# Performance work log

Measured on AMD Instinct MI355X. Metric: run time of the kernel, lower is better.

Reference implementation:

```python
import jax, jax.numpy as jnp
import numpy as np


def setup_inputs() -> dict:
    key = jax.random.key(0)
    ks = jax.random.split(key, 5)
    B, C, H, W = 4, 512, 64, 64
    A = 64  # attention_features
    s = lambda fan_in: 1.0 / np.sqrt(fan_in)
    return {
        "x": jax.random.normal(ks[0], (B, C, H, W), dtype=jnp.float32),
        "Wf": jax.random.normal(ks[1], (C, A), dtype=jnp.float32) * s(C),
        "bf": jnp.zeros((A,), dtype=jnp.float32),
        "Wg": jax.random.normal(ks[2], (C, A), dtype=jnp.float32) * s(C),
        "bg": jnp.zeros((A,), dtype=jnp.float32),
        "Wh": jax.random.normal(ks[3], (C, C), dtype=jnp.float32) * s(C),
        "bh": jnp.zeros((C,), dtype=jnp.float32),
        "scale": jax.random.uniform(ks[4], (), dtype=jnp.float32),
    }


def reference(x, Wf, bf, Wg, bg, Wh, bh, scale):
    B, C, H, W = x.shape
    N = H * W

    def conv1x1(w, b):  # 1x1 conv == per-pixel matmul over channels
        return jnp.einsum('bchw,cf->bfhw', x, w) + b[None, :, None, None]

    f = conv1x1(Wf, bf)  # [B, A, H, W]
    g = conv1x1(Wg, bg)  # [B, A, H, W]
    h = conv1x1(Wh, bh)  # [B, C, H, W]

    # flatten_hw (channels_first): [B, C', H, W] -> [B, N, C']
    flat = lambda t: t.reshape(B, t.shape[1], N).transpose(0, 2, 1)
    gf = flat(g)  # [B, N, A]
    ff = flat(f)  # [B, N, A]
    hf = flat(h)  # [B, N, C]

    s = jnp.einsum('bnd,bmd->bnm', gf, ff)       # [B, N, N]
    attn = jax.nn.softmax(s, axis=-1)
    o = jnp.einsum('bnm,bmc->bnc', attn, hf)     # [B, N, C]
    # Original does a raw reshape back to x's shape (no transpose) — keep it.
    y = scale * o.reshape(x.shape) + x
    return y
```

## Files before the change

### kernel.cpp

```cpp
#include <hip/hip_runtime.h>
#include <hip/hip_bf16.h>

constexpr int BB = 4;
constexpr int C  = 512;
constexpr int A  = 64;
constexpr int N  = 4096;

typedef __attribute__((ext_vector_type(8))) short s16x8;
typedef __attribute__((ext_vector_type(4))) float f32x4;

#define MFMA_16x16x32_BF16(a, b, c) __builtin_amdgcn_mfma_f32_16x16x32_bf16((a), (b), (c), 0, 0, 0)

typedef __attribute__((address_space(3))) unsigned int lds_u32_t;
typedef const __attribute__((address_space(1))) unsigned int glb_u32_t;

__device__ __forceinline__ void gl2lds16(const void* g, void* l) {
    __builtin_amdgcn_global_load_lds((glb_u32_t*)g, (lds_u32_t*)l, 16, 0, 0);
}

__global__ __launch_bounds__(256) void k_trans(const float* __restrict__ src,
                                               __hip_bfloat16* __restrict__ dst,
                                               int K, int M) {
    __shared__ __hip_bfloat16 Ls[64][66];
    int m0 = blockIdx.x << 6, k0 = blockIdx.y << 6;
    size_t bo = (size_t)blockIdx.z * K * M;
    int t = threadIdx.x;
    int lm = t & 63, g = t >> 6;
    #pragma unroll
    for (int j = 0; j < 16; ++j) {
        int kk = j * 4 + g;
        Ls[kk][lm] = __float2bfloat16(src[bo + (size_t)(k0 + kk) * M + m0 + lm]);
    }
    __syncthreads();
    #pragma unroll
    for (int j = 0; j < 16; ++j) {
        int mm = j * 4 + g;
        dst[bo + (size_t)(m0 + mm) * K + k0 + lm] = Ls[lm][mm];
    }
}

__global__ __launch_bounds__(256) void k_trans2(const float* __restrict__ src,
                                                __hip_bfloat16* __restrict__ dhi,
                                                __hip_bfloat16* __restrict__ dlo,
                                                int K, int M) {
    __shared__ float Ls[64][65];
    int m0 = blockIdx.x << 6, k0 = blockIdx.y << 6;
    size_t bo = (size_t)blockIdx.z * K * M;
    int t = threadIdx.x;
    int lm = t & 63, g = t >> 6;
    #pragma unroll
    for (int j = 0; j < 16; ++j) {
        int kk = j * 4 + g;
        Ls[kk][lm] = src[bo + (size_t)(k0 + kk) * M + m0 + lm];
    }
    __syncthreads();
    #pragma unroll
    for (int j = 0; j < 16; ++j) {
        int mm = j * 4 + g;
        float v = Ls[lm][mm];
        __hip_bfloat16 h = __float2bfloat16(v);
        size_t idx = bo + (size_t)(m0 + mm) * K + k0 + lm;
        dhi[idx] = h;
        dlo[idx] = __float2bfloat16(v - __bfloat162float(h));
    }
}

__global__ __launch_bounds__(256) void k_fgm(const __hip_bfloat16* __restrict__ XThi, const __hip_bfloat16* __restrict__ XTlo,
                                             const __hip_bfloat16* __restrict__ WfThi, const __hip_bfloat16* __restrict__ WfTlo,
                                             const __hip_bfloat16* __restrict__ WgThi, const __hip_bfloat16* __restrict__ WgTlo,
                                             const float* __restrict__ bfv, const float* __restrict__ bgv,
                                             __hip_bfloat16* __restrict__ FFhi, __hip_bfloat16* __restrict__ FFlo,
                                             __hip_bfloat16* __restrict__ GFhi, __hip_bfloat16* __restrict__ GFlo) {
    __shared__ __align__(16) __hip_bfloat16 Ah[64 * 32], Al[64 * 32];
    __shared__ __align__(16) __hip_bfloat16 Bh[128 * 32], Bl[128 * 32];
    int r0 = blockIdx.x << 6;
    int t = threadIdx.x;
    int w = t >> 6, l = t & 63;
    int ln15 = l & 15, quad = l >> 4;
    int mh = w & 1, nh = w >> 1;

    f32x4 acc[2][4];
    #pragma unroll
    for (int mi = 0; mi < 2; ++mi)
        #pragma unroll
        for (int ni = 0; ni < 4; ++ni) acc[mi][ni] = (f32x4){0.f, 0.f, 0.f, 0.f};

    for (int kt = 0; kt < C; kt += 32) {
        {
            int row = t >> 2, seg = t & 3;
            int gseg = (seg - (row >> 1)) & 3;
            size_t go = (size_t)(r0 + row) * C + kt + gseg * 8;
            gl2lds16(XThi + go, &Ah[t * 8]);
            gl2lds16(XTlo + go, &Al[t * 8]);
        }
        #pragma unroll
        for (int j = 0; j < 2; ++j) {
            int i = j * 256 + t;
            int row = i >> 2, seg = i & 3;
            int gseg = (seg - (row >> 1)) & 3;
            size_t go = (size_t)(row & 63) * C + kt + gseg * 8;
            const __hip_bfloat16* bh = j ? WgThi : WfThi;
            const __hip_bfloat16* bl = j ? WgTlo : WfTlo;
            gl2lds16(bh + go, &Bh[i * 8]);
            gl2lds16(bl + go, &Bl[i * 8]);
        }
        __syncthreads();
        s16x8 afh[2], afl[2], bfh[4], bfl[4];
        #pragma unroll
        for (int mi = 0; mi < 2; ++mi) {
            int row = mh * 32 + mi * 16 + ln15;
            int sw = ((quad + (row >> 1)) & 3) << 3;
            afh[mi] = *(const s16x8*)&Ah[row * 32 + sw];
            afl[mi] = *(const s16x8*)&Al[row * 32 + sw];
        }
        #pragma unroll
        for (int ni = 0; ni < 4; ++ni) {
            int row = nh * 64 + ni * 16 + ln15;
            int sw = ((quad + (row >> 1)) & 3) << 3;
            bfh[ni] = *(const s16x8*)&Bh[row * 32 + sw];
            bfl[ni] = *(const s16x8*)&Bl[row * 32 + sw];
        }
        #pragma unroll
        for (int mi = 0; mi < 2; ++mi)
            #pragma unroll
            for (int ni = 0; ni < 4; ++ni) {
                acc[mi][ni] = MFMA_16x16x32_BF16(afh[mi], bfh[ni], acc[mi][ni]);
                acc[mi][ni] = MFMA_16x16x32_BF16(afl[mi], bfh[ni], acc[mi][ni]);
                acc[mi][ni] = MFMA_16x16x32_BF16(afh[mi], bfl[ni], acc[mi][ni]);
            }
        __syncthreads();
    }

    #pragma unroll
    for (int mi = 0; mi < 2; ++mi) {
        #pragma unroll
        for (int r = 0; r < 4; ++r) {
            size_t grow = (size_t)(r0 + mh * 32 + mi * 16 + quad * 4 + r) * A;
            #pragma unroll
            for (int ni = 0; ni < 4; ++ni) {
                int col = nh * 64 + ni * 16 + ln15;
                if (col < A) {
                    float v = acc[mi][ni][r] + bfv[col];
                    __hip_bfloat16 h = __float2bfloat16(v);
                    FFhi[grow + col] = h;
                    FFlo[grow + col] = __float2bfloat16(v - __bfloat162float(h));
                } else {
                    int a = col - A;
                    float v = acc[mi][ni][r] + bgv[a];
                    __hip_bfloat16 h = __float2bfloat16(v);
                    GFhi[grow + a] = h;
                    GFlo[grow + a] = __float2bfloat16(v - __bfloat162float(h));
                }
            }
        }
    }
}

__global__ __launch_bounds__(256) void k_hm(const __hip_bfloat16* __restrict__ WhT,
                                            const __hip_bfloat16* __restrict__ XT,
                                            const float* __restrict__ bhv,
                                            __hip_bfloat16* __restrict__ HFT) {
    __shared__ __align__(16) __hip_bfloat16 As[128 * 32];
    __shared__ __align__(16) __hip_bfloat16 Bs[128 * 32];
    int b  = blockIdx.z;
    int c0 = blockIdx.x << 7;
    int n0 = blockIdx.y << 7;
    int t = threadIdx.x;
    int w = t >> 6, l = t & 63;
    int ln15 = l & 15, quad = l >> 4;
    int mc = (w >> 1) << 6, nn = (w & 1) << 6;

    const __hip_bfloat16* Bb = XT + (size_t)b * N * C;

    f32x4 acc[4][4];
    #pragma unroll
    for (int mi = 0; mi < 4; ++mi)
        #pragma unroll
        for (int ni = 0; ni < 4; ++ni) acc[mi][ni] = (f32x4){0.f, 0.f, 0.f, 0.f};

    for (int kt = 0; kt < C; kt += 32) {
        #pragma unroll
        for (int j = 0; j < 2; ++j) {
            int i = j * 256 + t;
            int row = i >> 2, seg = i & 3;
            int gseg = (seg - (row >> 1)) & 3;
            gl2lds16(WhT + ((size_t)(c0 + row) * C + kt + gseg * 8), &As[i * 8]);
        }
        #pragma unroll
        for (int j = 0; j < 2; ++j) {
            int i = j * 256 + t;
            int row = i >> 2, seg = i & 3;
            int gseg = (seg - (row >> 1)) & 3;
            gl2lds16(Bb + ((size_t)(n0 + row) * C + kt + gseg * 8), &Bs[i * 8]);
        }
        __syncthreads();
        s16x8 af[4], bf2[4];
        #pragma unroll
        for (int mi = 0; mi < 4; ++mi) {
            int row = mc + mi * 16 + ln15;
            int sw = ((quad + (row >> 1)) & 3) << 3;
            af[mi] = *(const s16x8*)&As[row * 32 + sw];
        }
        #pragma unroll
        for (int ni = 0; ni < 4; ++ni) {
            int row = nn + ni * 16 + ln15;
            int sw = ((quad + (row >> 1)) & 3) << 3;
            bf2[ni] = *(const s16x8*)&Bs[row * 32 + sw];
        }
        #pragma unroll
        for (int mi = 0; mi < 4; ++mi)
            #pragma unroll
            for (int ni = 0; ni < 4; ++ni)
                acc[mi][ni] = MFMA_16x16x32_BF16(af[mi], bf2[ni], acc[mi][ni]);
        __syncthreads();
    }

    #pragma unroll
    for (int mi = 0; mi < 4; ++mi) {
        #pragma unroll
        for (int r = 0; r < 4; ++r) {
            int c = c0 + mc + mi * 16 + quad * 4 + r;
            float bias = bhv[c];
            size_t rowbase = ((size_t)b * C + c) * N;
            #pragma unroll
            for (int ni = 0; ni < 4; ++ni) {
                int n = n0 + nn + ni * 16 + ln15;
                HFT[rowbase + n] = __float2bfloat16(acc[mi][ni][r] + bias);
            }
        }
    }
}

__global__ __launch_bounds__(512) void k_s(const __hip_bfloat16* __restrict__ GFhi, const __hip_bfloat16* __restrict__ GFlo,
                                           const __hip_bfloat16* __restrict__ FFhi, const __hip_bfloat16* __restrict__ FFlo,
                                           __hip_bfloat16* __restrict__ P, float* __restrict__ rowsum) {
    __shared__ __align__(16) __hip_bfloat16 Fsh[2][128 * 32];
    __shared__ __align__(16) __hip_bfloat16 Fsl[2][128 * 32];
    __shared__ float sred[8][32];
    int b = blockIdx.y;
    int q0 = blockIdx.x << 6;
    int t = threadIdx.x;
    int w = t >> 6, l = t & 63;
    int ln15 = l & 15, quad = l >> 4, q8 = quad << 3;
    int qh = w & 1, kq = w >> 1;
    int qbase = q0 + qh * 32;

    const __hip_bfloat16* Fh = FFhi + (size_t)b * N * A;
    const __hip_bfloat16* Fl = FFlo + (size_t)b * N * A;
    __hip_bfloat16* Pb = P + (size_t)b * N * N;

    s16x8 ah[2][2], al[2][2];
    #pragma unroll
    for (int m = 0; m < 2; ++m) {
        const __hip_bfloat16* gp = GFhi + ((size_t)(b * N + qbase + m * 16 + ln15)) * A + q8;
        const __hip_bfloat16* lp = GFlo + ((size_t)(b * N + qbase + m * 16 + ln15)) * A + q8;
        ah[m][0] = *(const s16x8*)gp; ah[m][1] = *(const s16x8*)(gp + 32);
        al[m][0] = *(const s16x8*)lp; al[m][1] = *(const s16x8*)(lp + 32);
    }

    int srow = t >> 2;
    int sseg = ((t & 3) - (srow >> 1)) & 3;
    size_t sgoff0 = (size_t)srow * A + sseg * 8;

    float sm[2][4] = {{0.f,0.f,0.f,0.f},{0.f,0.f,0.f,0.f}};
    for (int kt = 0; kt < N; kt += 128) {
        gl2lds16(Fh + (size_t)kt * A + sgoff0,      &Fsh[0][t * 8]);
        gl2lds16(Fh + (size_t)kt * A + 32 + sgoff0, &Fsh[1][t * 8]);
        gl2lds16(Fl + (size_t)kt * A + sgoff0,      &Fsl[0][t * 8]);
        gl2lds16(Fl + (size_t)kt * A + 32 + sgoff0, &Fsl[1][t * 8]);
        __syncthreads();
        #pragma unroll
        for (int s = 0; s < 2; ++s) {
            int sub = kq * 2 + s;
            int ro = sub * 16 + ln15;
            int sw = ((quad + (ro >> 1)) & 3) << 3;
            s16x8 kh0 = *(const s16x8*)&Fsh[0][ro * 32 + sw];
            s16x8 kh1 = *(const s16x8*)&Fsh[1][ro * 32 + sw];
            s16x8 kl0 = *(const s16x8*)&Fsl[0][ro * 32 + sw];
            s16x8 kl1 = *(const s16x8*)&Fsl[1][ro * 32 + sw];
            int key = kt + sub * 16 + ln15;
            #pragma unroll
            for (int m = 0; m < 2; ++m) {
                f32x4 acc = {0.f, 0.f, 0.f, 0.f};
                acc = MFMA_16x16x32_BF16(ah[m][0], kh0, acc);
                acc = MFMA_16x16x32_BF16(ah[m][1], kh1, acc);
                acc = MFMA_16x16x32_BF16(al[m][0], kh0, acc);
                acc = MFMA_16x16x32_BF16(al[m][1], kh1, acc);
                acc = MFMA_16x16x32_BF16(ah[m][0], kl0, acc);
                acc = MFMA_16x16x32_BF16(ah[m][1], kl1, acc);
                size_t prow = (size_t)(qbase + m * 16 + quad * 4) * N + key;
                #pragma unroll
                for (int r = 0; r < 4; ++r) {
                    float p = __expf(acc[r]);
                    __hip_bfloat16 pb = __float2bfloat16(p);
                    sm[m][r] += __bfloat162float(pb);
                    Pb[prow + (size_t)r * N] = pb;
                }
            }
        }
        __syncthreads();
    }
    #pragma unroll
    for (int d = 1; d < 16; d <<= 1)
        #pragma unroll
        for (int m = 0; m < 2; ++m)
            #pragma unroll
            for (int r = 0; r < 4; ++r) sm[m][r] += __shfl_xor(sm[m][r], d, 64);
    if (ln15 == 0) {
        #pragma unroll
        for (int m = 0; m < 2; ++m)
            #pragma unroll
            for (int r = 0; r < 4; ++r) sred[w][m * 16 + quad * 4 + r] = sm[m][r];
    }
    __syncthreads();
    if (t < 64) {
        int hq = t >> 5, row = t & 31;
        rowsum[b * N + q0 + t] = sred[hq][row] + sred[hq + 2][row] +
                                 sred[hq + 4][row] + sred[hq + 6][row];
    }
}

__global__ __launch_bounds__(256) void k_o(const __hip_bfloat16* __restrict__ P,
                                           const __hip_bfloat16* __restrict__ HFT,
                                           const float* __restrict__ rowsum,
                                           const float* __restrict__ x,
                                           const float* __restrict__ scalep,
                                           float* __restrict__ out) {
    __shared__ __align__(16) __hip_bfloat16 As[128 * 32];
    __shared__ __align__(16) __hip_bfloat16 Bs[128 * 32];
    int id = blockIdx.x;
    int cb   = (id >> 3) & 3;
    int rest = (id & 7) | ((id >> 5) << 3);
    int qs = rest & 31, b = rest >> 5;
    int q0 = qs << 7, c0 = cb << 7;
    int t = threadIdx.x;
    int w = t >> 6, l = t & 63;
    int ln15 = l & 15, quad = l >> 4;
    int mq = (w >> 1) << 6, nc = (w & 1) << 6;

    const __hip_bfloat16* Ab = P   + (size_t)b * N * N;
    const __hip_bfloat16* Bb = HFT + (size_t)b * C * N;

    f32x4 acc[4][4];
    #pragma unroll
    for (int mi = 0; mi < 4; ++mi)
        #pragma unroll
        for (int ni = 0; ni < 4; ++ni) acc[mi][ni] = (f32x4){0.f, 0.f, 0.f, 0.f};

    for (int kt = 0; kt < N; kt += 32) {
        #pragma unroll
        for (int j = 0; j < 2; ++j) {
            int i = j * 256 + t;
            int row = i >> 2, seg = i & 3;
            int gseg = (seg - (row >> 1)) & 3;
            gl2lds16(Ab + ((size_t)(q0 + row) * N + kt + gseg * 8), &As[i * 8]);
        }
        #pragma unroll
        for (int j = 0; j < 2; ++j) {
            int i = j * 256 + t;
            int row = i >> 2, seg = i & 3;
            int gseg = (seg - (row >> 1)) & 3;
            gl2lds16(Bb + ((size_t)(c0 + row) * N + kt + gseg * 8), &Bs[i * 8]);
        }
        __syncthreads();
        s16x8 af[4], bf2[4];
        #pragma unroll
        for (int mi = 0; mi < 4; ++mi) {
            int row = mq + mi * 16 + ln15;
            int sw = ((quad + (row >> 1)) & 3) << 3;
            af[mi] = *(const s16x8*)&As[row * 32 + sw];
        }
        #pragma unroll
        for (int ni = 0; ni < 4; ++ni) {
            int row = nc + ni * 16 + ln15;
            int sw = ((quad + (row >> 1)) & 3) << 3;
            bf2[ni] = *(const s16x8*)&Bs[row * 32 + sw];
        }
        #pragma unroll
        for (int mi = 0; mi < 4; ++mi)
            #pragma unroll
            for (int ni = 0; ni < 4; ++ni)
                acc[mi][ni] = MFMA_16x16x32_BF16(af[mi], bf2[ni], acc[mi][ni]);
        __syncthreads();
    }

    float scv = *scalep;
    #pragma unroll
    for (int mi = 0; mi < 4; ++mi) {
        #pragma unroll
        for (int r = 0; r < 4; ++r) {
            int q = q0 + mq + mi * 16 + quad * 4 + r;
            float srs = scv / rowsum[b * N + q];
            size_t rowbase = (size_t)b * N * C + (size_t)q * C;
            #pragma unroll
            for (int ni = 0; ni < 4; ++ni) {
                size_t idx = rowbase + (size_t)(c0 + nc + ni * 16 + ln15);
                out[idx] = acc[mi][ni][r] * srs + x[idx];
            }
        }
    }
}

extern "C" void kernel_launch(void* const* d_in, const int* in_sizes, int n_in,
                              void* d_out, int out_size, void* d_ws, size_t ws_size,
                              hipStream_t stream) {
    const float* x   = (const float*)d_in[0];
    const float* Wf  = (const float*)d_in[1];
    const float* bfv = (const float*)d_in[2];
    const float* Wg  = (const float*)d_in[3];
    const float* bgv = (const float*)d_in[4];
    const float* Wh  = (const float*)d_in[5];
    const float* bhv = (const float*)d_in[6];
    const float* sc  = (const float*)d_in[7];
    float* out = (float*)d_out;

    char* ws = (char*)d_ws;
    size_t off = 0;
    __hip_bfloat16* FFhi = (__hip_bfloat16*)(ws + off); off += (size_t)BB * N * A * 2;
    __hip_bfloat16* FFlo = (__hip_bfloat16*)(ws + off); off += (size_t)BB * N * A * 2;
    __hip_bfloat16* GFhi = (__hip_bfloat16*)(ws + off); off += (size_t)BB * N * A * 2;
    __hip_bfloat16* GFlo = (__hip_bfloat16*)(ws + off); off += (size_t)BB * N * A * 2;
    __hip_bfloat16* HFT  = (__hip_bfloat16*)(ws + off); off += (size_t)BB * C * N * 2;
    char* Pbase          = (ws + off);                  off += (size_t)BB * N * N * 2;
    __hip_bfloat16* P    = (__hip_bfloat16*)Pbase;
    float* rowsum        = (float*)(ws + off);          off += (size_t)BB * N * 4;
    __hip_bfloat16* WhT  = (__hip_bfloat16*)(ws + off); off += (size_t)C * C * 2;
    __hip_bfloat16* WfThi = (__hip_bfloat16*)(ws + off); off += (size_t)A * C * 2;
    __hip_bfloat16* WfTlo = (__hip_bfloat16*)(ws + off); off += (size_t)A * C * 2;
    __hip_bfloat16* WgThi = (__hip_bfloat16*)(ws + off); off += (size_t)A * C * 2;
    __hip_bfloat16* WgTlo = (__hip_bfloat16*)(ws + off); off += (size_t)A * C * 2;
    __hip_bfloat16* XThi = (__hip_bfloat16*)(Pbase + (size_t)BB * N * N * 2 - (size_t)BB * N * C * 2);
    __hip_bfloat16* XTlo = (__hip_bfloat16*)(Pbase + (size_t)BB * N * N * 2 - 2 * (size_t)BB * N * C * 2);

    k_trans<<<dim3(C / 64, C / 64, 1), dim3(256), 0, stream>>>(Wh, WhT, C, C);
    k_trans2<<<dim3(N / 64, C / 64, BB), dim3(256), 0, stream>>>(x, XThi, XTlo, C, N);
    k_trans2<<<dim3(A / 64, C / 64, 1), dim3(256), 0, stream>>>(Wf, WfThi, WfTlo, C, A);
    k_trans2<<<dim3(A / 64, C / 64, 1), dim3(256), 0, stream>>>(Wg, WgThi, WgTlo, C, A);
    k_hm<<<dim3(C / 128, N / 128, BB), dim3(256), 0, stream>>>(WhT, XThi, bhv, HFT);
    k_fgm<<<dim3((BB * N) / 64), dim3(256), 0, stream>>>(XThi, XTlo, WfThi, WfTlo, WgThi, WgTlo,
                                                         bfv, bgv, FFhi, FFlo, GFhi, GFlo);
    k_s<<<dim3(N / 64, BB), dim3(512), 0, stream>>>(GFhi, GFlo, FFhi, FFlo, P, rowsum);
    k_o<<<dim3(512), dim3(256), 0, stream>>>(P, HFT, rowsum, x, sc, out);
}
```

Baseline: 290.6 us.

## Fuse score/exp and P·H matmul into one flash-style kernel, drop P buffer

Replaces the separate score kernel (which wrote the full N×N exp matrix to global memory) and the output GEMM kernel with a single kernel. Each block handles 32 queries across all 512 channels, computes exp scores for 64 keys into LDS, then immediately multiplies them with H loaded straight from global into registers. This removes the 128 MB write and re-read of P and one launch. In exchange each block re-reads all of F and H per 32 queries, with no LDS staging for H and only 512 blocks. There is also no running max, matching the old unnormalised exp scheme.

After: 479.2 us. +64.9%, slower.

```diff
diff --git a/kernel.cpp b/kernel.cpp
--- a/kernel.cpp
+++ b/kernel.cpp
@@ -231,170 +231,127 @@
     }
 }
 
-__global__ __launch_bounds__(512) void k_s(const __hip_bfloat16* __restrict__ GFhi, const __hip_bfloat16* __restrict__ GFlo,
-                                           const __hip_bfloat16* __restrict__ FFhi, const __hip_bfloat16* __restrict__ FFlo,
-                                           __hip_bfloat16* __restrict__ P, float* __restrict__ rowsum) {
-    __shared__ __align__(16) __hip_bfloat16 Fsh[2][128 * 32];
-    __shared__ __align__(16) __hip_bfloat16 Fsl[2][128 * 32];
-    __shared__ float sred[8][32];
-    int b = blockIdx.y;
-    int q0 = blockIdx.x << 6;
+__global__ __launch_bounds__(256) void k_so(const __hip_bfloat16* __restrict__ GFhi, const __hip_bfloat16* __restrict__ GFlo,
+                                            const __hip_bfloat16* __restrict__ FFhi, const __hip_bfloat16* __restrict__ FFlo,
+                                            const __hip_bfloat16* __restrict__ HFT,
+                                            const float* __restrict__ x,
+                                            const float* __restrict__ scalep,
+                                            float* __restrict__ out) {
+    __shared__ __align__(16) __hip_bfloat16 Pl[32 * 64];
+    __shared__ float sred[4][32];
+    __shared__ float rsum[32];
+
+    int id  = blockIdx.x;
+    int xcd = id & 7;
+    int b   = xcd >> 1;
+    int qs  = ((id >> 3) << 1) | (xcd & 1);
+    int q0  = qs << 5;
+
     int t = threadIdx.x;
     int w = t >> 6, l = t & 63;
     int ln15 = l & 15, quad = l >> 4, q8 = quad << 3;
-    int qh = w & 1, kq = w >> 1;
-    int qbase = q0 + qh * 32;
 
     const __hip_bfloat16* Fh = FFhi + (size_t)b * N * A;
     const __hip_bfloat16* Fl = FFlo + (size_t)b * N * A;
-    __hip_bfloat16* Pb = P + (size_t)b * N * N;
+    const __hip_bfloat16* Hb = HFT  + (size_t)b * C * N;
 
     s16x8 ah[2][2], al[2][2];
     #pragma unroll
-    for (int m = 0; m < 2; ++m) {
-        const __hip_bfloat16* gp = GFhi + ((size_t)(b * N + qbase + m * 16 + ln15)) * A + q8;
-        const __hip_bfloat16* lp = GFlo + ((size_t)(b * N + qbase + m * 16 + ln15)) * A + q8;
-        ah[m][0] = *(const s16x8*)gp; ah[m][1] = *(const s16x8*)(gp + 32);
-        al[m][0] = *(const s16x8*)lp; al[m][1] = *(const s16x8*)(lp + 32);
-    }
-
-    int srow = t >> 2;
-    int sseg = ((t & 3) - (srow >> 1)) & 3;
-    size_t sgoff0 = (size_t)srow * A + sseg * 8;
-
+    for (int mi = 0; mi < 2; ++mi) {
+        const __hip_bfloat16* gp = GFhi + (size_t)(b * N + q0 + mi * 16 + ln15) * A + q8;
+        const __hip_bfloat16* lp = GFlo + (size_t)(b * N + q0 + mi * 16 + ln15) * A + q8;
+        ah[mi][0] = *(const s16x8*)gp; ah[mi][1] = *(const s16x8*)(gp + 32);
+        al[mi][0] = *(const s16x8*)lp; al[mi][1] = *(const s16x8*)(lp + 32);
+    }
+
+    f32x4 acc[2][8];
+    #pragma unroll
+    for (int mi = 0; mi < 2; ++mi)
+        #pragma unroll
+        for (int ni = 0; ni < 8; ++ni) acc[mi][ni] = (f32x4){0.f, 0.f, 0.f, 0.f};
     float sm[2][4] = {{0.f,0.f,0.f,0.f},{0.f,0.f,0.f,0.f}};
-    for (int kt = 0; kt < N; kt += 128) {
-        gl2lds16(Fh + (size_t)kt * A + sgoff0,      &Fsh[0][t * 8]);
-        gl2lds16(Fh + (size_t)kt * A + 32 + sgoff0, &Fsh[1][t * 8]);
-        gl2lds16(Fl + (size_t)kt * A + sgoff0,      &Fsl[0][t * 8]);
-        gl2lds16(Fl + (size_t)kt * A + 32 + sgoff0, &Fsl[1][t * 8]);
-        __syncthreads();
-        #pragma unroll
-        for (int s = 0; s < 2; ++s) {
-            int sub = kq * 2 + s;
-            int ro = sub * 16 + ln15;
-            int sw = ((quad + (ro >> 1)) & 3) << 3;
-            s16x8 kh0 = *(const s16x8*)&Fsh[0][ro * 32 + sw];
-            s16x8 kh1 = *(const s16x8*)&Fsh[1][ro * 32 + sw];
-            s16x8 kl0 = *(const s16x8*)&Fsl[0][ro * 32 + sw];
-            s16x8 kl1 = *(const s16x8*)&Fsl[1][ro * 32 + sw];
-            int key = kt + sub * 16 + ln15;
-            #pragma unroll
-            for (int m = 0; m < 2; ++m) {
-                f32x4 acc = {0.f, 0.f, 0.f, 0.f};
-                acc = MFMA_16x16x32_BF16(ah[m][0], kh0, acc);
-                acc = MFMA_16x16x32_BF16(ah[m][1], kh1, acc);
-                acc = MFMA_16x16x32_BF16(al[m][0], kh0, acc);
-                acc = MFMA_16x16x32_BF16(al[m][1], kh1, acc);
-                acc = MFMA_16x16x32_BF16(ah[m][0], kl0, acc);
-                acc = MFMA_16x16x32_BF16(ah[m][1], kl1, acc);
-                size_t prow = (size_t)(qbase + m * 16 + quad * 4) * N + key;
+
+    char* Pb = (char*)&Pl[0];
+
+    for (int kt = 0; kt < N; kt += 64) {
+        const __hip_bfloat16* fr  = Fh + (size_t)(kt + w * 16 + ln15) * A + q8;
+        const __hip_bfloat16* flr = Fl + (size_t)(kt + w * 16 + ln15) * A + q8;
+        s16x8 kh0 = *(const s16x8*)fr;
+        s16x8 kh1 = *(const s16x8*)(fr + 32);
+        s16x8 kl0 = *(const s16x8*)flr;
+        s16x8 kl1 = *(const s16x8*)(flr + 32);
+        s16x8 hb[2][8];
+        #pragma unroll
+        for (int ks = 0; ks < 2; ++ks)
+            #pragma unroll
+            for (int ni = 0; ni < 8; ++ni)
+                hb[ks][ni] = *(const s16x8*)&Hb[(size_t)(w * 128 + ni * 16 + ln15) * N + kt + ks * 32 + q8];
+        #pragma unroll
+        for (int mi = 0; mi < 2; ++mi) {
+            f32x4 s = {0.f, 0.f, 0.f, 0.f};
+            s = MFMA_16x16x32_BF16(ah[mi][0], kh0, s);
+            s = MFMA_16x16x32_BF16(ah[mi][1], kh1, s);
+            s = MFMA_16x16x32_BF16(al[mi][0], kh0, s);
+            s = MFMA_16x16x32_BF16(al[mi][1], kh1, s);
+            s = MFMA_16x16x32_BF16(ah[mi][0], kl0, s);
+            s = MFMA_16x16x32_BF16(ah[mi][1], kl1, s);
+            int key2 = (w * 16 + ln15) << 1;
+            #pragma unroll
+            for (int r = 0; r < 4; ++r) {
+                int q = mi * 16 + quad * 4 + r;
+                float p = __expf(s[r]);
+                __hip_bfloat16 pb = __float2bfloat16(p);
+                sm[mi][r] += __bfloat162float(pb);
+                *(__hip_bfloat16*)(Pb + q * 128 + (key2 ^ ((q & 7) << 4))) = pb;
+            }
+        }
+        __syncthreads();
+        #pragma unroll
+        for (int ks = 0; ks < 2; ++ks) {
+            s16x8 pa[2];
+            #pragma unroll
+            for (int mi = 0; mi < 2; ++mi) {
+                int q = mi * 16 + ln15;
+                pa[mi] = *(const s16x8*)(Pb + q * 128 + ((ks * 64 + quad * 16) ^ ((q & 7) << 4)));
+            }
+            #pragma unroll
+            for (int mi = 0; mi < 2; ++mi)
                 #pragma unroll
-                for (int r = 0; r < 4; ++r) {
-                    float p = __expf(acc[r]);
-                    __hip_bfloat16 pb = __float2bfloat16(p);
-                    sm[m][r] += __bfloat162float(pb);
-                    Pb[prow + (size_t)r * N] = pb;
-                }
-            }
-        }
-        __syncthreads();
-    }
-    #pragma unroll
-    for (int d = 1; d < 16; d <<= 1)
-        #pragma unroll
-        for (int m = 0; m < 2; ++m)
-            #pragma unroll
-            for (int r = 0; r < 4; ++r) sm[m][r] += __shfl_xor(sm[m][r], d, 64);
+                for (int ni = 0; ni < 8; ++ni)
+                    acc[mi][ni] = MFMA_16x16x32_BF16(pa[mi], hb[ks][ni], acc[mi][ni]);
+        }
+        __syncthreads();
+    }
+
+    #pragma unroll
+    for (int mi = 0; mi < 2; ++mi)
+        #pragma unroll
+        for (int r = 0; r < 4; ++r)
+            #pragma unroll
+            for (int d = 1; d < 16; d <<= 1)
+                sm[mi][r] += __shfl_xor(sm[mi][r], d, 64);
     if (ln15 == 0) {
         #pragma unroll
-        for (int m = 0; m < 2; ++m)
-            #pragma unroll
-            for (int r = 0; r < 4; ++r) sred[w][m * 16 + quad * 4 + r] = sm[m][r];
+        for (int mi = 0; mi < 2; ++mi)
+            #pragma unroll
+            for (int r = 0; r < 4; ++r)
+                sred[w][mi * 16 + quad * 4 + r] = sm[mi][r];
     }
     __syncthreads();
-    if (t < 64) {
-        int hq = t >> 5, row = t & 31;
-        rowsum[b * N + q0 + t] = sred[hq][row] + sred[hq + 2][row] +
-                                 sred[hq + 4][row] + sred[hq + 6][row];
-    }
-}
-
-__global__ __launch_bounds__(256) void k_o(const __hip_bfloat16* __restrict__ P,
-                                           const __hip_bfloat16* __restrict__ HFT,
-                                           const float* __restrict__ rowsum,
-                                           const float* __restrict__ x,
-                                           const float* __restrict__ scalep,
-                                           float* __restrict__ out) {
-    __shared__ __align__(16) __hip_bfloat16 As[128 * 32];
-    __shared__ __align__(16) __hip_bfloat16 Bs[128 * 32];
-    int id = blockIdx.x;
-    int cb   = (id >> 3) & 3;
-    int rest = (id & 7) | ((id >> 5) << 3);
-    int qs = rest & 31, b = rest >> 5;
-    int q0 = qs << 7, c0 = cb << 7;
-    int t = threadIdx.x;
-    int w = t >> 6, l = t & 63;
-    int ln15 = l & 15, quad = l >> 4;
-    int mq = (w >> 1) << 6, nc = (w & 1) << 6;
-
-    const __hip_bfloat16* Ab = P   + (size_t)b * N * N;
-    const __hip_bfloat16* Bb = HFT + (size_t)b * C * N;
-
-    f32x4 acc[4][4];
-    #pragma unroll
-    for (int mi = 0; mi < 4; ++mi)
-        #pragma unroll
-        for (int ni = 0; ni < 4; ++ni) acc[mi][ni] = (f32x4){0.f, 0.f, 0.f, 0.f};
-
-    for (int kt = 0; kt < N; kt += 32) {
-        #pragma unroll
-        for (int j = 0; j < 2; ++j) {
-            int i = j * 256 + t;
-            int row = i >> 2, seg = i & 3;
-            int gseg = (seg - (row >> 1)) & 3;
-            gl2lds16(Ab + ((size_t)(q0 + row) * N + kt + gseg * 8), &As[i * 8]);
-        }
-        #pragma unroll
-        for (int j = 0; j < 2; ++j) {
-            int i = j * 256 + t;
-            int row = i >> 2, seg = i & 3;
-            int gseg = (seg - (row >> 1)) & 3;
-            gl2lds16(Bb + ((size_t)(c0 + row) * N + kt + gseg * 8), &Bs[i * 8]);
-        }
-        __syncthreads();
-        s16x8 af[4], bf2[4];
-        #pragma unroll
-        for (int mi = 0; mi < 4; ++mi) {
-            int row = mq + mi * 16 + ln15;
-            int sw = ((quad + (row >> 1)) & 3) << 3;
-            af[mi] = *(const s16x8*)&As[row * 32 + sw];
-        }
-        #pragma unroll
-        for (int ni = 0; ni < 4; ++ni) {
-            int row = nc + ni * 16 + ln15;
-            int sw = ((quad + (row >> 1)) & 3) << 3;
-            bf2[ni] = *(const s16x8*)&Bs[row * 32 + sw];
-        }
-        #pragma unroll
-        for (int mi = 0; mi < 4; ++mi)
-            #pragma unroll
-            for (int ni = 0; ni < 4; ++ni)
-                acc[mi][ni] = MFMA_16x16x32_BF16(af[mi], bf2[ni], acc[mi][ni]);
-        __syncthreads();
-    }
+    if (t < 32) rsum[t] = sred[0][t] + sred[1][t] + sred[2][t] + sred[3][t];
+    __syncthreads();
 
     float scv = *scalep;
     #pragma unroll
-    for (int mi = 0; mi < 4; ++mi) {
+    for (int mi = 0; mi < 2; ++mi) {
         #pragma unroll
         for (int r = 0; r < 4; ++r) {
-            int q = q0 + mq + mi * 16 + quad * 4 + r;
-            float srs = scv / rowsum[b * N + q];
-            size_t rowbase = (size_t)b * N * C + (size_t)q * C;
-            #pragma unroll
-            for (int ni = 0; ni < 4; ++ni) {
-                size_t idx = rowbase + (size_t)(c0 + nc + ni * 16 + ln15);
+            int q = mi * 16 + quad * 4 + r;
+            float srs = scv / rsum[q];
+            size_t rowbase = (size_t)(b * N + q0 + q) * C;
+            #pragma unroll
+            for (int ni = 0; ni < 8; ++ni) {
+                size_t idx = rowbase + w * 128 + ni * 16 + ln15;
                 out[idx] = acc[mi][ni][r] * srs + x[idx];
             }
         }
@@ -422,8 +379,7 @@
     __hip_bfloat16* GFlo = (__hip_bfloat16*)(ws + off); off += (size_t)BB * N * A * 2;
     __hip_bfloat16* HFT  = (__hip_bfloat16*)(ws + off); off += (size_t)BB * C * N * 2;
     char* Pbase          = (ws + off);                  off += (size_t)BB * N * N * 2;
-    __hip_bfloat16* P    = (__hip_bfloat16*)Pbase;
-    float* rowsum        = (float*)(ws + off);          off += (size_t)BB * N * 4;
+    off += (size_t)BB * N * 4;
     __hip_bfloat16* WhT  = (__hip_bfloat16*)(ws + off); off += (size_t)C * C * 2;
     __hip_bfloat16* WfThi = (__hip_bfloat16*)(ws + off); off += (size_t)A * C * 2;
     __hip_bfloat16* WfTlo = (__hip_bfloat16*)(ws + off); off += (size_t)A * C * 2;
@@ -439,6 +395,5 @@
     k_hm<<<dim3(C / 128, N / 128, BB), dim3(256), 0, stream>>>(WhT, XThi, bhv, HFT);
     k_fgm<<<dim3((BB * N) / 64), dim3(256), 0, stream>>>(XThi, XTlo, WfThi, WfTlo, WgThi, WgTlo,
                                                          bfv, bgv, FFhi, FFlo, GFhi, GFlo);
-    k_s<<<dim3(N / 64, BB), dim3(512), 0, stream>>>(GFhi, GFlo, FFhi, FFlo, P, rowsum);
-    k_o<<<dim3(512), dim3(256), 0, stream>>>(P, HFT, rowsum, x, sc, out);
-}
+    k_so<<<dim3(BB * (N / 32)), dim3(256), 0, stream>>>(GFhi, GFlo, FFhi, FFlo, HFT, x, sc, out);
+}
```
